# Optimization experiments

Hardware: AMD Instinct MI355X
Metric: run time of the kernel (lower is better)

Reference implementation:

```python
import jax, jax.numpy as jnp
import numpy as np

N, E, DIN, DH = 50000, 1600000, 128, 128
P_DROP = 0.5


def setup_inputs() -> dict:
    key = jax.random.key(0)
    ks = jax.random.split(key, 9)
    scale = 0.05
    x = jax.random.normal(ks[0], (N, DIN), jnp.float32)
    edge_index = jax.random.randint(ks[1], (2, E), 0, N, dtype=jnp.int32)
    W0 = jax.random.normal(ks[2], (DH, DIN), jnp.float32) * scale
    b0 = jnp.zeros((DH,), jnp.float32)
    W1 = jax.random.normal(ks[3], (DH, DH), jnp.float32) * scale
    b1 = jnp.zeros((DH,), jnp.float32)
    W2 = jax.random.normal(ks[4], (DH, DH), jnp.float32) * scale
    b2 = jnp.zeros((DH,), jnp.float32)
    # deterministic inverted-dropout mask (train-mode Dropout(p=0.5))
    drop_mask = jax.random.bernoulli(ks[5], 1.0 - P_DROP, (N, DH)).astype(jnp.float32) / (1.0 - P_DROP)
    return {"x": x, "edge_index": edge_index, "drop_mask": drop_mask,
            "W0": W0, "b0": b0, "W1": W1, "b1": b1, "W2": W2, "b2": b2}


def _gcn_conv(h_in, W, b, src, dst, dinv):
    # PyG GCNConv: linear -> symmetric-normalized aggregation with self loops -> bias
    h = h_in @ W.T                                   # [N, out]
    norm = dinv[src] * dinv[dst]                      # [E]
    msg = h[src] * norm[:, None]                      # [E, out]
    out = jax.ops.segment_sum(msg, dst, num_segments=N)
    out = out + h * (dinv * dinv)[:, None]            # self-loop contribution
    return out + b


def reference(x, edge_index, drop_mask, W0, b0, W1, b1, W2, b2):
    src, dst = edge_index[0], edge_index[1]
    # degree of target nodes, +1 for the added self loop (shared by all layers)
    deg = jax.ops.segment_sum(jnp.ones((E,), x.dtype), dst, num_segments=N) + 1.0
    dinv = jax.lax.rsqrt(deg)

    h = _gcn_conv(x, W0, b0, src, dst, dinv)
    h = jax.nn.relu(h * drop_mask)                    # Dropout(0.5) then ReLU
    x_ = _gcn_conv(h, W1, b1, src, dst, dinv)
    x2 = _gcn_conv(h, W2, b2, src, dst, dinv)         # conv2 also consumes h (as in source)
    return (x_, x2)
```

## Files before the change

kernel.cpp:

```cpp
#include <hip/hip_runtime.h>


#define D 128
#define BK_SHIFT 7
#define BK_NODES 128
#define NBMAX 512
#define CAP 7936
#define TILE_A 2048

typedef __attribute__((ext_vector_type(8))) short bf16x8;
typedef __attribute__((ext_vector_type(4))) float f32x4;

static __device__ __forceinline__ unsigned f2bf(float f) {
  union { float f; unsigned u; } v; v.f = f;
  unsigned r = v.u + 0x7FFF + ((v.u >> 16) & 1);
  return r >> 16;
}
static __device__ __forceinline__ float bflo(unsigned u) {
  return __uint_as_float(u << 16);
}
static __device__ __forceinline__ float bfhi(unsigned u) {
  return __uint_as_float(u & 0xFFFF0000u);
}


__global__ __launch_bounds__(256) void k_bucketA(const int* __restrict__ src,
                                                 const int* __restrict__ dst,
                                                 int* __restrict__ bcnt,
                                                 int* __restrict__ packed,
                                                 int E, int nb) {
  __shared__ int hist[NBMAX];
  __shared__ int base[NBMAX];
  __shared__ unsigned pv[TILE_A];
  int t = threadIdx.x;
  int e0 = blockIdx.x * TILE_A;

  for (int b = t; b < nb; b += 256) hist[b] = 0;
  __syncthreads();

  for (int i = t; i < TILE_A; i += 256) {
    int e = e0 + i;
    if (e < E) {
      int d = dst[e];
      int s = src[e];
      unsigned bkt = (unsigned)d >> BK_SHIFT;
      pv[i] = (unsigned)(s & 0xFFFF) | ((unsigned)(d & (BK_NODES - 1)) << 16) |
              (bkt << 23);
      atomicAdd(&hist[bkt], 1);
    }
  }
  __syncthreads();

  for (int b = t; b < nb; b += 256) {
    int h = hist[b];
    if (h) base[b] = atomicAdd(&bcnt[b], h);
  }
  __syncthreads();

  for (int i = t; i < TILE_A; i += 256) {
    int e = e0 + i;
    if (e < E) {
      unsigned v = pv[i];
      unsigned bkt = v >> 23;
      int pos = atomicAdd(&base[bkt], 1);
      if (pos < CAP) packed[(size_t)bkt * CAP + pos] = (int)(v & 0x7FFFFF);
    }
  }
}

__global__ __launch_bounds__(512) void k_bucketB2(const int* __restrict__ packed,
                                                  const int* __restrict__ bcnt,
                                                  int* __restrict__ srcSorted,
                                                  int* __restrict__ rowBeg,
                                                  int* __restrict__ rowEnd,
                                                  float* __restrict__ dinv,
                                                  int n) {
  __shared__ int histC[BK_NODES];
  __shared__ int cur[BK_NODES];
  __shared__ int buf[CAP];
  int t = threadIdx.x;
  int bkt = blockIdx.x;
  int n0 = bkt << BK_SHIFT;
  int beg = bkt * CAP;
  int cnt = bcnt[bkt];
  if (cnt > CAP) cnt = CAP;

  if (t < BK_NODES) histC[t] = 0;
  __syncthreads();

  for (int i = t; i < cnt; i += 512)
    atomicAdd(&histC[packed[beg + i] >> 16], 1);
  __syncthreads();

  if (t == 0) {
    int run = 0;
#pragma unroll
    for (int j = 0; j < BK_NODES; ++j) { cur[j] = run; run += histC[j]; }
  }
  __syncthreads();

  if (t < BK_NODES && n0 + t < n) {
    int rb = beg + cur[t];
    rowBeg[n0 + t] = rb;
    rowEnd[n0 + t] = rb + histC[t];
    dinv[n0 + t]   = rsqrtf((float)histC[t] + 1.0f);
  }
  __syncthreads();

  for (int i = t; i < cnt; i += 512) {
    int p = packed[beg + i];
    int pos = atomicAdd(&cur[p >> 16], 1);
    buf[pos] = p & 0xFFFF;
  }
  __syncthreads();
  for (int i = t; i < cnt; i += 512)
    srcSorted[beg + i] = buf[i] << 8;
}


template <int EPI>
__global__ __launch_bounds__(256) void k_aggb(const unsigned* __restrict__ T,
                                              const int* __restrict__ srcSorted,
                                              const int* __restrict__ rowBeg,
                                              const int* __restrict__ rowEnd,
                                              const float* __restrict__ dinv,
                                              const float* __restrict__ bias,
                                              const float* __restrict__ mask,
                                              unsigned* __restrict__ outB,
                                              int n) {
  int wave = (blockIdx.x * 256 + threadIdx.x) >> 6;
  int lane = threadIdx.x & 63;
  if (wave >= n) return;
  const char* Tb = (const char*)T;
  int lo = lane << 2;
  int beg = rowBeg[wave], end = rowEnd[wave];
  float a0x = 0.f, a0y = 0.f, a1x = 0.f, a1y = 0.f;
  float a2x = 0.f, a2y = 0.f, a3x = 0.f, a3y = 0.f;
  int j = beg;
  for (; j + 15 < end; j += 16) {
    unsigned u[16];
#pragma unroll
    for (int q = 0; q < 16; ++q) {
      int off = __builtin_nontemporal_load(srcSorted + j + q);
      u[q] = *(const unsigned*)(Tb + off + lo);
    }
#pragma unroll
    for (int q = 0; q < 16; q += 4) {
      a0x += bflo(u[q + 0]);  a0y += bfhi(u[q + 0]);
      a1x += bflo(u[q + 1]);  a1y += bfhi(u[q + 1]);
      a2x += bflo(u[q + 2]);  a2y += bfhi(u[q + 2]);
      a3x += bflo(u[q + 3]);  a3y += bfhi(u[q + 3]);
    }
  }
  for (; j + 7 < end; j += 8) {
    unsigned u[8];
#pragma unroll
    for (int q = 0; q < 8; ++q) {
      int off = __builtin_nontemporal_load(srcSorted + j + q);
      u[q] = *(const unsigned*)(Tb + off + lo);
    }
#pragma unroll
    for (int q = 0; q < 8; q += 4) {
      a0x += bflo(u[q + 0]);  a0y += bfhi(u[q + 0]);
      a1x += bflo(u[q + 1]);  a1y += bfhi(u[q + 1]);
      a2x += bflo(u[q + 2]);  a2y += bfhi(u[q + 2]);
      a3x += bflo(u[q + 3]);  a3y += bfhi(u[q + 3]);
    }
  }
  for (; j < end; ++j) {
    int off = __builtin_nontemporal_load(srcSorted + j);
    unsigned u = *(const unsigned*)(Tb + off + lo);
    a0x += bflo(u);
    a0y += bfhi(u);
  }
  unsigned us = T[(size_t)wave * 64 + lane];
  float dn = dinv[wave];
  float ox = ((a0x + a1x) + (a2x + a3x) + bflo(us)) * dn;
  float oy = ((a0y + a1y) + (a2y + a3y) + bfhi(us)) * dn;
  if (EPI == 1) {
    float2 bv = ((const float2*)bias)[lane];
    float2 mv = ((const float2*)mask)[(size_t)wave * 64 + lane];
    float hx = fmaxf((ox + bv.x) * mv.x, 0.f);
    float hy = fmaxf((oy + bv.y) * mv.y, 0.f);
    outB[(size_t)wave * 64 + lane] = f2bf(hx * dn) | (f2bf(hy * dn) << 16);
  } else {
    outB[(size_t)wave * 64 + lane] = f2bf(ox) | (f2bf(oy) << 16);
  }
}


__global__ __launch_bounds__(256) void k_wcvt(const float* __restrict__ W0,
                                              const float* __restrict__ W1,
                                              const float* __restrict__ W2,
                                              unsigned short* __restrict__ out) {
  int i = blockIdx.x * 256 + threadIdx.x;
  if (i >= 3 * 16384) return;
  const float* W = (i < 16384) ? W0 : (i < 32768 ? W1 : W2);
  out[i] = (unsigned short)f2bf(W[i & 16383]);
}


template <bool BF16IN, bool BF16OUT>
__global__ __launch_bounds__(256) void k_gemm_mfma(const void* __restrict__ Xv,
                                                   const unsigned short* __restrict__ Wb,
                                                   const float* __restrict__ bias,
                                                   const float* __restrict__ prescale,
                                                   float* __restrict__ Cf,
                                                   unsigned short* __restrict__ Cb,
                                                   int nrows) {
  int wid  = threadIdx.x >> 6;
  int lane = threadIdx.x & 63;
  int r0   = blockIdx.x * 64 + wid * 16;
  int arow = r0 + (lane & 15);
  int kb   = (lane >> 4) * 8;
  bool rowok = arow < nrows;

  bf16x8 a[4];
  if (BF16IN) {
    const unsigned short* X = (const unsigned short*)Xv;
#pragma unroll
    for (int ks = 0; ks < 4; ++ks) {
      bf16x8 t;
      if (rowok) t = *reinterpret_cast<const bf16x8*>(X + (size_t)arow * D + ks * 32 + kb);
      else { for (int q = 0; q < 8; ++q) t[q] = 0; }
      a[ks] = t;
    }
  } else {
    const float* X = (const float*)Xv;
#pragma unroll
    for (int ks = 0; ks < 4; ++ks) {
      bf16x8 t;
      if (rowok) {
        const float* p = X + (size_t)arow * D + ks * 32 + kb;
        float4 f0 = *(const float4*)(p);
        float4 f1 = *(const float4*)(p + 4);
        t[0] = (short)f2bf(f0.x); t[1] = (short)f2bf(f0.y);
        t[2] = (short)f2bf(f0.z); t[3] = (short)f2bf(f0.w);
        t[4] = (short)f2bf(f1.x); t[5] = (short)f2bf(f1.y);
        t[6] = (short)f2bf(f1.z); t[7] = (short)f2bf(f1.w);
      } else {
        for (int q = 0; q < 8; ++q) t[q] = 0;
      }
      a[ks] = t;
    }
  }

  int rbase = r0 + (lane >> 4) * 4;
  float sc[4];
  if (BF16OUT) {
#pragma unroll
    for (int reg = 0; reg < 4; ++reg) {
      int rr = rbase + reg;
      sc[reg] = (prescale && rr < nrows) ? prescale[rr] : 1.0f;
    }
  }

#pragma unroll
  for (int ct = 0; ct < 8; ++ct) {
    int col = ct * 16 + (lane & 15);
    f32x4 acc = {0.f, 0.f, 0.f, 0.f};
#pragma unroll
    for (int ks = 0; ks < 4; ++ks) {
      bf16x8 b = *reinterpret_cast<const bf16x8*>(Wb + (size_t)col * D + ks * 32 + kb);
      acc = __builtin_amdgcn_mfma_f32_16x16x32_bf16(a[ks], b, acc, 0, 0, 0);
    }
    if (BF16OUT) {
#pragma unroll
      for (int reg = 0; reg < 4; ++reg) {
        int rr = rbase + reg;
        if (rr < nrows)
          Cb[(size_t)rr * D + col] = (unsigned short)f2bf(acc[reg] * sc[reg]);
      }
    } else {
      float bc = bias ? bias[col] : 0.f;
#pragma unroll
      for (int reg = 0; reg < 4; ++reg) {
        int rr = rbase + reg;
        if (rr < nrows) Cf[(size_t)rr * D + col] = acc[reg] + bc;
      }
    }
  }
}

__global__ __launch_bounds__(256) void k_gemm_mfma2(const unsigned short* __restrict__ X,
                                                    const unsigned short* __restrict__ W1b,
                                                    const unsigned short* __restrict__ W2b,
                                                    const float* __restrict__ b1,
                                                    const float* __restrict__ b2,
                                                    float* __restrict__ C1,
                                                    float* __restrict__ C2,
                                                    int nrows) {
  int wid  = threadIdx.x >> 6;
  int lane = threadIdx.x & 63;
  int r0   = blockIdx.x * 64 + wid * 16;
  int arow = r0 + (lane & 15);
  int kb   = (lane >> 4) * 8;
  bool rowok = arow < nrows;

  bf16x8 a[4];
#pragma unroll
  for (int ks = 0; ks < 4; ++ks) {
    bf16x8 t;
    if (rowok) t = *reinterpret_cast<const bf16x8*>(X + (size_t)arow * D + ks * 32 + kb);
    else { for (int q = 0; q < 8; ++q) t[q] = 0; }
    a[ks] = t;
  }

  int rbase = r0 + (lane >> 4) * 4;

#pragma unroll
  for (int wm = 0; wm < 2; ++wm) {
    const unsigned short* Wb = (wm == 0) ? W1b : W2b;
    const float* bias        = (wm == 0) ? b1 : b2;
    float* Cf                = (wm == 0) ? C1 : C2;
#pragma unroll
    for (int ct = 0; ct < 8; ++ct) {
      int col = ct * 16 + (lane & 15);
      f32x4 acc = {0.f, 0.f, 0.f, 0.f};
#pragma unroll
      for (int ks = 0; ks < 4; ++ks) {
        bf16x8 b = *reinterpret_cast<const bf16x8*>(Wb + (size_t)col * D + ks * 32 + kb);
        acc = __builtin_amdgcn_mfma_f32_16x16x32_bf16(a[ks], b, acc, 0, 0, 0);
      }
      float bc = bias[col];
#pragma unroll
      for (int reg = 0; reg < 4; ++reg) {
        int rr = rbase + reg;
        if (rr < nrows) Cf[(size_t)rr * D + col] = acc[reg] + bc;
      }
    }
  }
}


__global__ __launch_bounds__(256) void k_deg_f(const int* __restrict__ dst,
                                               float* __restrict__ deg, int E) {
  int i = blockIdx.x * 256 + threadIdx.x;
  if (i < E) atomicAdd(&deg[dst[i]], 1.0f);
}

__global__ __launch_bounds__(256) void k_dinv_f(float* __restrict__ deg, int n) {
  int i = blockIdx.x * 256 + threadIdx.x;
  if (i < n) deg[i] = rsqrtf(deg[i] + 1.0f);
}

__global__ __launch_bounds__(256) void k_selfmul(const float* __restrict__ X,
                                                 const float* __restrict__ dinv,
                                                 float* __restrict__ out, int n) {
  int i = blockIdx.x * 256 + threadIdx.x;
  if (i >= n * 32) return;
  int r = i >> 5, c4 = (i & 31) << 2;
  float di = dinv[r];
  float s = di * di;
  float4 h = *(const float4*)(X + (size_t)r * D + c4);
  h.x *= s; h.y *= s; h.z *= s; h.w *= s;
  *(float4*)(out + (size_t)r * D + c4) = h;
}

__global__ __launch_bounds__(256) void k_relumask(float* __restrict__ h,
                                                  const float* __restrict__ mask, int n) {
  int i = blockIdx.x * 256 + threadIdx.x;
  if (i >= n * 32) return;
  float4 v = *(const float4*)(h + (size_t)i * 4);
  float4 m = *(const float4*)(mask + (size_t)i * 4);
  v.x = fmaxf(v.x * m.x, 0.f);
  v.y = fmaxf(v.y * m.y, 0.f);
  v.z = fmaxf(v.z * m.z, 0.f);
  v.w = fmaxf(v.w * m.w, 0.f);
  *(float4*)(h + (size_t)i * 4) = v;
}

__global__ __launch_bounds__(256) void k_aggatomic(const float* __restrict__ X,
                                                   const int* __restrict__ src,
                                                   const int* __restrict__ dst,
                                                   const float* __restrict__ dinv,
                                                   float* __restrict__ out, int E) {
  int gid = blockIdx.x * 256 + threadIdx.x;
  int wave = gid >> 6;
  int lane = threadIdx.x & 63;
  int nw = (gridDim.x * 256) >> 6;
  for (int e = wave; e < E; e += nw) {
    int s = src[e], d = dst[e];
    float nrm = dinv[s] * dinv[d];
    float2 v = ((const float2*)(X + (size_t)s * D))[lane];
    float* op = out + (size_t)d * D + lane * 2;
    atomicAdd(op, v.x * nrm);
    atomicAdd(op + 1, v.y * nrm);
  }
}

__global__ __launch_bounds__(256) void k_addbias(float* __restrict__ C,
                                                 const float* __restrict__ bias, int n) {
  int i = blockIdx.x * 256 + threadIdx.x;
  if (i >= n * 32) return;
  int c4 = (i & 31) << 2;
  float4 v = *(const float4*)(C + (size_t)i * 4);
  float4 b = *(const float4*)(bias + c4);
  v.x += b.x; v.y += b.y; v.z += b.z; v.w += b.w;
  *(float4*)(C + (size_t)i * 4) = v;
}

template <bool BF16OUT>
__global__ __launch_bounds__(256) void k_gemm128(const float* __restrict__ X,
                                                 const float* __restrict__ W,
                                                 const float* __restrict__ bias,
                                                 const float* __restrict__ prescale,
                                                 float* __restrict__ Cf,
                                                 unsigned short* __restrict__ Cb,
                                                 int nrows) {
  __shared__ float Xs[64][132];
  __shared__ float Ws[32][128];

  int tid = threadIdx.x;
  int row0 = blockIdx.x * 64;

  for (int t = tid; t < 2048; t += 256) {
    int r = t >> 5;
    int c4 = (t & 31) << 2;
    int gr = row0 + r;
    float4 v = make_float4(0.f, 0.f, 0.f, 0.f);
    if (gr < nrows) v = *(const float4*)(X + (size_t)gr * D + c4);
    Xs[r][c4 + 0] = v.x; Xs[r][c4 + 1] = v.y;
    Xs[r][c4 + 2] = v.z; Xs[r][c4 + 3] = v.w;
  }

  float acc[4][8];
#pragma unroll
  for (int i = 0; i < 4; ++i)
#pragma unroll
    for (int j = 0; j < 8; ++j) acc[i][j] = 0.f;

  int ty = tid >> 4, tx = tid & 15;
  int r0 = ty << 2, c0 = tx << 3;

  for (int k0 = 0; k0 < 128; k0 += 32) {
    int j = tid >> 1;
    int kkb = (tid & 1) << 4;
    const float4* wp = (const float4*)(W + j * D + k0 + kkb);
    float4 wa = wp[0], wb = wp[1], wc = wp[2], wd = wp[3];

    __syncthreads();
    Ws[kkb +  0][j] = wa.x; Ws[kkb +  1][j] = wa.y; Ws[kkb +  2][j] = wa.z; Ws[kkb +  3][j] = wa.w;
    Ws[kkb +  4][j] = wb.x; Ws[kkb +  5][j] = wb.y; Ws[kkb +  6][j] = wb.z; Ws[kkb +  7][j] = wb.w;
    Ws[kkb +  8][j] = wc.x; Ws[kkb +  9][j] = wc.y; Ws[kkb + 10][j] = wc.z; Ws[kkb + 11][j] = wc.w;
    Ws[kkb + 12][j] = wd.x; Ws[kkb + 13][j] = wd.y; Ws[kkb + 14][j] = wd.z; Ws[kkb + 15][j] = wd.w;
    __syncthreads();

#pragma unroll
    for (int kk = 0; kk < 32; ++kk) {
      float xi[4];
      xi[0] = Xs[r0 + 0][k0 + kk];
      xi[1] = Xs[r0 + 1][k0 + kk];
      xi[2] = Xs[r0 + 2][k0 + kk];
      xi[3] = Xs[r0 + 3][k0 + kk];
      float4 wv0 = *(const float4*)(&Ws[kk][c0]);
      float4 wv1 = *(const float4*)(&Ws[kk][c0 + 4]);
      float wf[8] = {wv0.x, wv0.y, wv0.z, wv0.w, wv1.x, wv1.y, wv1.z, wv1.w};
#pragma unroll
      for (int i = 0; i < 4; ++i)
#pragma unroll
        for (int jj = 0; jj < 8; ++jj) acc[i][jj] += xi[i] * wf[jj];
    }
  }

  float4 bv0 = make_float4(0.f, 0.f, 0.f, 0.f);
  float4 bv1 = make_float4(0.f, 0.f, 0.f, 0.f);
  if (bias) {
    bv0 = *(const float4*)(bias + c0);
    bv1 = *(const float4*)(bias + c0 + 4);
  }

#pragma unroll
  for (int i = 0; i < 4; ++i) {
    int gr = row0 + r0 + i;
    if (gr < nrows) {
      float o[8];
      o[0] = acc[i][0] + bv0.x; o[1] = acc[i][1] + bv0.y;
      o[2] = acc[i][2] + bv0.z; o[3] = acc[i][3] + bv0.w;
      o[4] = acc[i][4] + bv1.x; o[5] = acc[i][5] + bv1.y;
      o[6] = acc[i][6] + bv1.z; o[7] = acc[i][7] + bv1.w;
      if (BF16OUT) {
        float dn = prescale ? prescale[gr] : 1.0f;
        uint4 pk;
        pk.x = f2bf(o[0] * dn) | (f2bf(o[1] * dn) << 16);
        pk.y = f2bf(o[2] * dn) | (f2bf(o[3] * dn) << 16);
        pk.z = f2bf(o[4] * dn) | (f2bf(o[5] * dn) << 16);
        pk.w = f2bf(o[6] * dn) | (f2bf(o[7] * dn) << 16);
        *(uint4*)(Cb + (size_t)gr * D + c0) = pk;
      } else {
        *(float4*)(Cf + (size_t)gr * D + c0)     = make_float4(o[0], o[1], o[2], o[3]);
        *(float4*)(Cf + (size_t)gr * D + c0 + 4) = make_float4(o[4], o[5], o[6], o[7]);
      }
    }
  }
}


extern "C" void kernel_launch(void* const* d_in, const int* in_sizes, int n_in,
                              void* d_out, int out_size, void* d_ws, size_t ws_size,
                              hipStream_t stream) {
  const float* x    = (const float*)d_in[0];
  const int*   ei   = (const int*)d_in[1];
  const float* mask = (const float*)d_in[2];
  const float* W0   = (const float*)d_in[3];
  const float* b0   = (const float*)d_in[4];
  const float* W1   = (const float*)d_in[5];
  const float* b1   = (const float*)d_in[6];
  const float* W2   = (const float*)d_in[7];
  const float* b2   = (const float*)d_in[8];

  const int N = in_sizes[0] / D;
  const int E = in_sizes[1] / 2;
  const int* srcv = ei;
  const int* dstv = ei + E;

  float* out  = (float*)d_out;
  float* outA = out;
  float* outB = out + (size_t)N * D;

  const size_t featBytes  = (size_t)N * D * sizeof(float);
  const size_t featBytesH = (size_t)N * D * sizeof(short);
  const int gGemm  = (N + 63) / 64;
  const int gEdge  = (E + 255) / 256;
  const int gNode  = (N + 255) / 256;
  const int gWaveN = (N + 3) / 4;
  const int gElem  = (N * 32 + 255) / 256;
  const int nb     = (N + BK_NODES - 1) >> BK_SHIFT;
  const int gBA    = (E + TILE_A - 1) / TILE_A;
  const size_t padBytes = (size_t)nb * CAP * 4;

  auto align256 = [](size_t v) { return (v + 255) & ~(size_t)255; };
  char* w = (char*)d_ws;
  size_t off = 0;
  int*   bcnt      = (int*)(w + off);   off = align256(off + NBMAX * 4);
  int*   rowBeg    = (int*)(w + off);   off = align256(off + (size_t)N * 4);
  int*   rowEnd    = (int*)(w + off);   off = align256(off + (size_t)N * 4);
  float* dinv      = (float*)(w + off); off = align256(off + (size_t)N * 4);
  int*   srcSorted = (int*)(w + off);   off = align256(off + padBytes);
  unsigned short* Wb = (unsigned short*)(w + off); off = align256(off + 3 * 16384 * 2);
  unsigned* h0bf   = (unsigned*)(w + off); off = align256(off + featBytesH);
  unsigned* hbf    = (unsigned*)(w + off); off = align256(off + featBytesH);
  unsigned* gbf    = (unsigned*)(w + off); off = align256(off + featBytesH);
  int*   packed    = (int*)gbf;
  size_t need = off;

  if (ws_size >= need && N <= 65536 && nb <= NBMAX &&
      padBytes <= featBytesH && (E / nb) + 1024 <= CAP) {
    hipMemsetAsync(bcnt, 0, (size_t)nb * sizeof(int), stream);
    k_bucketA<<<gBA, 256, 0, stream>>>(srcv, dstv, bcnt, packed, E, nb);
    k_bucketB2<<<nb, 512, 0, stream>>>(packed, bcnt, srcSorted, rowBeg,
                                       rowEnd, dinv, N);
    k_wcvt<<<192, 256, 0, stream>>>(W0, W1, W2, Wb);

    k_gemm_mfma<false, true><<<gGemm, 256, 0, stream>>>(
        x, Wb, nullptr, dinv, nullptr, (unsigned short*)h0bf, N);
    k_aggb<1><<<gWaveN, 256, 0, stream>>>(h0bf, srcSorted, rowBeg, rowEnd,
                                          dinv, b0, mask, hbf, N);
    k_aggb<2><<<gWaveN, 256, 0, stream>>>(hbf, srcSorted, rowBeg, rowEnd,
                                          dinv, nullptr, nullptr, gbf, N);
    k_gemm_mfma2<<<gGemm, 256, 0, stream>>>(
        (const unsigned short*)gbf, Wb + 16384, Wb + 32768, b1, b2,
        outA, outB, N);
  } else {
    float* fdinv = (float*)(w);
    float* fA    = (float*)(w + 0x40000);
    float* fB    = (float*)((char*)fA + featBytes);
    hipMemsetAsync(fdinv, 0, (size_t)N * sizeof(float), stream);
    k_deg_f<<<gEdge, 256, 0, stream>>>(dstv, fdinv, E);
    k_dinv_f<<<gNode, 256, 0, stream>>>(fdinv, N);
    k_gemm128<false><<<gGemm, 256, 0, stream>>>(x, W0, nullptr, nullptr, fB, nullptr, N);
    k_selfmul<<<gElem, 256, 0, stream>>>(fB, fdinv, fA, N);
    k_aggatomic<<<4096, 256, 0, stream>>>(fB, srcv, dstv, fdinv, fA, E);
    k_addbias<<<gElem, 256, 0, stream>>>(fA, b0, N);
    k_relumask<<<gElem, 256, 0, stream>>>(fA, mask, N);
    k_selfmul<<<gElem, 256, 0, stream>>>(fA, fdinv, fB, N);
    k_aggatomic<<<4096, 256, 0, stream>>>(fA, srcv, dstv, fdinv, fB, E);
    k_gemm128<false><<<gGemm, 256, 0, stream>>>(fB, W1, b1, nullptr, outA, nullptr, N);
    k_gemm128<false><<<gGemm, 256, 0, stream>>>(fB, W2, b2, nullptr, outB, nullptr, N);
  }
}
```

Measured before the change: 236.8 us.

## Compact sorted edge list, fuse weight conversion into bucketing, drop nontemporal loads

Bucket B now reserves a contiguous output range per bucket through a global atomic counter, so srcSorted is a dense E-length array instead of a padded per-bucket layout with CAP stride. The weight bf16 conversion kernel is folded into the first 192 blocks of the bucketing kernel, removing one launch. The aggregation kernel reads edge indices with ordinary loads instead of nontemporal ones, so they can be cached. Bucket order in the compacted array becomes nondeterministic, but it is still correct because each node keeps contiguous row bounds.

```diff
diff --git a/kernel.cpp b/kernel.cpp
--- a/kernel.cpp
+++ b/kernel.cpp
@@ -28,12 +28,22 @@
                                                  const int* __restrict__ dst,
                                                  int* __restrict__ bcnt,
                                                  int* __restrict__ packed,
+                                                 const float* __restrict__ W0,
+                                                 const float* __restrict__ W1,
+                                                 const float* __restrict__ W2,
+                                                 unsigned short* __restrict__ Wb,
                                                  int E, int nb) {
   __shared__ int hist[NBMAX];
   __shared__ int base[NBMAX];
   __shared__ unsigned pv[TILE_A];
   int t = threadIdx.x;
   int e0 = blockIdx.x * TILE_A;
+
+  if (blockIdx.x < 192) {
+    int i = blockIdx.x * 256 + t;
+    const float* W = (i < 16384) ? W0 : (i < 32768 ? W1 : W2);
+    Wb[i] = (unsigned short)f2bf(W[i & 16383]);
+  }
 
   for (int b = t; b < nb; b += 256) hist[b] = 0;
   __syncthreads();
@@ -70,6 +80,7 @@
 
 __global__ __launch_bounds__(512) void k_bucketB2(const int* __restrict__ packed,
                                                   const int* __restrict__ bcnt,
+                                                  int* __restrict__ gcur,
                                                   int* __restrict__ srcSorted,
                                                   int* __restrict__ rowBeg,
                                                   int* __restrict__ rowEnd,
@@ -78,6 +89,7 @@
   __shared__ int histC[BK_NODES];
   __shared__ int cur[BK_NODES];
   __shared__ int buf[CAP];
+  __shared__ int obase;
   int t = threadIdx.x;
   int bkt = blockIdx.x;
   int n0 = bkt << BK_SHIFT;
@@ -96,11 +108,12 @@
     int run = 0;
 #pragma unroll
     for (int j = 0; j < BK_NODES; ++j) { cur[j] = run; run += histC[j]; }
+    obase = atomicAdd(gcur, run);
   }
   __syncthreads();
 
   if (t < BK_NODES && n0 + t < n) {
-    int rb = beg + cur[t];
+    int rb = obase + cur[t];
     rowBeg[n0 + t] = rb;
     rowEnd[n0 + t] = rb + histC[t];
     dinv[n0 + t]   = rsqrtf((float)histC[t] + 1.0f);
@@ -114,7 +127,7 @@
   }
   __syncthreads();
   for (int i = t; i < cnt; i += 512)
-    srcSorted[beg + i] = buf[i] << 8;
+    srcSorted[obase + i] = buf[i] << 8;
 }
 
 
@@ -140,10 +153,8 @@
   for (; j + 15 < end; j += 16) {
     unsigned u[16];
 #pragma unroll
-    for (int q = 0; q < 16; ++q) {
-      int off = __builtin_nontemporal_load(srcSorted + j + q);
-      u[q] = *(const unsigned*)(Tb + off + lo);
-    }
+    for (int q = 0; q < 16; ++q)
+      u[q] = *(const unsigned*)(Tb + srcSorted[j + q] + lo);
 #pragma unroll
     for (int q = 0; q < 16; q += 4) {
       a0x += bflo(u[q + 0]);  a0y += bfhi(u[q + 0]);
@@ -155,10 +166,8 @@
   for (; j + 7 < end; j += 8) {
     unsigned u[8];
 #pragma unroll
-    for (int q = 0; q < 8; ++q) {
-      int off = __builtin_nontemporal_load(srcSorted + j + q);
-      u[q] = *(const unsigned*)(Tb + off + lo);
-    }
+    for (int q = 0; q < 8; ++q)
+      u[q] = *(const unsigned*)(Tb + srcSorted[j + q] + lo);
 #pragma unroll
     for (int q = 0; q < 8; q += 4) {
       a0x += bflo(u[q + 0]);  a0y += bfhi(u[q + 0]);
@@ -168,8 +177,7 @@
     }
   }
   for (; j < end; ++j) {
-    int off = __builtin_nontemporal_load(srcSorted + j);
-    unsigned u = *(const unsigned*)(Tb + off + lo);
+    unsigned u = *(const unsigned*)(Tb + srcSorted[j] + lo);
     a0x += bflo(u);
     a0y += bfhi(u);
   }
@@ -186,17 +194,6 @@
   } else {
     outB[(size_t)wave * 64 + lane] = f2bf(ox) | (f2bf(oy) << 16);
   }
-}
-
-
-__global__ __launch_bounds__(256) void k_wcvt(const float* __restrict__ W0,
-                                              const float* __restrict__ W1,
-                                              const float* __restrict__ W2,
-                                              unsigned short* __restrict__ out) {
-  int i = blockIdx.x * 256 + threadIdx.x;
-  if (i >= 3 * 16384) return;
-  const float* W = (i < 16384) ? W0 : (i < 32768 ? W1 : W2);
-  out[i] = (unsigned short)f2bf(W[i & 16383]);
 }
 
 
@@ -532,25 +529,31 @@
   auto align256 = [](size_t v) { return (v + 255) & ~(size_t)255; };
   char* w = (char*)d_ws;
   size_t off = 0;
-  int*   bcnt      = (int*)(w + off);   off = align256(off + NBMAX * 4);
+  int*   bcnt      = (int*)(w + off);   off = align256(off + (NBMAX + 1) * 4);
+  int*   gcur      = bcnt + NBMAX;
   int*   rowBeg    = (int*)(w + off);   off = align256(off + (size_t)N * 4);
   int*   rowEnd    = (int*)(w + off);   off = align256(off + (size_t)N * 4);
   float* dinv      = (float*)(w + off); off = align256(off + (size_t)N * 4);
-  int*   srcSorted = (int*)(w + off);   off = align256(off + padBytes);
+  int*   srcSorted = (int*)(w + off);   off = align256(off + (size_t)E * 4);
   unsigned short* Wb = (unsigned short*)(w + off); off = align256(off + 3 * 16384 * 2);
   unsigned* h0bf   = (unsigned*)(w + off); off = align256(off + featBytesH);
   unsigned* hbf    = (unsigned*)(w + off); off = align256(off + featBytesH);
-  unsigned* gbf    = (unsigned*)(w + off); off = align256(off + featBytesH);
+  size_t gbfOff    = off;
+  unsigned* gbf    = (unsigned*)(w + off);
+  size_t offA = off + featBytesH;
+  size_t offB = off + padBytes;
+  off = align256(offA > offB ? offA : offB);
   int*   packed    = (int*)gbf;
   size_t need = off;
+  (void)gbfOff;
 
   if (ws_size >= need && N <= 65536 && nb <= NBMAX &&
-      padBytes <= featBytesH && (E / nb) + 1024 <= CAP) {
-    hipMemsetAsync(bcnt, 0, (size_t)nb * sizeof(int), stream);
-    k_bucketA<<<gBA, 256, 0, stream>>>(srcv, dstv, bcnt, packed, E, nb);
-    k_bucketB2<<<nb, 512, 0, stream>>>(packed, bcnt, srcSorted, rowBeg,
-                                       rowEnd, dinv, N);
-    k_wcvt<<<192, 256, 0, stream>>>(W0, W1, W2, Wb);
+      (E / nb) + 1024 <= CAP) {
+    hipMemsetAsync(bcnt, 0, (size_t)(NBMAX + 1) * sizeof(int), stream);
+    k_bucketA<<<gBA, 256, 0, stream>>>(srcv, dstv, bcnt, packed,
+                                       W0, W1, W2, Wb, E, nb);
+    k_bucketB2<<<nb, 512, 0, stream>>>(packed, bcnt, gcur, srcSorted,
+                                       rowBeg, rowEnd, dinv, N);
 
     k_gemm_mfma<false, true><<<gGemm, 256, 0, stream>>>(
         x, Wb, nullptr, dinv, nullptr, (unsigned short*)h0bf, N);
```

After: 223.5 us. 1.06x faster.
